# Optimization experiments

Hardware: AMD Instinct MI355X
Metric: run time of the kernel (lower is better)

## Reference

```python
import jax, jax.numpy as jnp
import numpy as np

N, E, D, H, C = 50000, 800000, 64, 2, 64


def setup_inputs() -> dict:
    key = jax.random.key(0)
    ks = jax.random.split(key, 16)
    sc = 1.0 / np.sqrt(D)
    return {
        "left_features": jax.random.normal(ks[0], (N, D), jnp.float32),
        "edge_index": jax.random.randint(ks[1], (2, E), 0, N, jnp.int32),
        "edge_features": jax.random.normal(ks[2], (E, D), jnp.float32),
        "right_features": jax.random.normal(ks[3], (N, D), jnp.float32),
        "scatter_out_size": N,
        # GATConv params (shared lin for src/dst since in_channels is int)
        "W_lin": jax.random.normal(ks[4], (D, H * C), jnp.float32) * sc,
        "att_src": jax.random.normal(ks[5], (H, C), jnp.float32) * sc,
        "att_dst": jax.random.normal(ks[6], (H, C), jnp.float32) * sc,
        "W_edge": jax.random.normal(ks[7], (D, H * C), jnp.float32) * sc,
        "att_edge": jax.random.normal(ks[8], (H, C), jnp.float32) * sc,
        "bias_conv": jnp.zeros((H * C,), jnp.float32),
        # trailing dense layers
        "W_lt": jax.random.normal(ks[9], (H * C, C), jnp.float32) * sc,
        "b_lt": jnp.zeros((C,), jnp.float32),
        "W_fm": jax.random.normal(ks[10], (C, C), jnp.float32) * sc,
        "b_fm": jnp.zeros((C,), jnp.float32),
        "W_pc": jax.random.normal(ks[11], (2 * C, C), jnp.float32) * sc,
        "b_pc": jnp.zeros((C,), jnp.float32),
    }


def reference(left_features, edge_index, edge_features, right_features,
              scatter_out_size, W_lin, att_src, att_dst, W_edge, att_edge,
              bias_conv, W_lt, b_lt, W_fm, b_fm, W_pc, b_pc):
    src, dst = edge_index[0], edge_index[1]
    Nl = scatter_out_size
    # linear projections to [*, H, C]
    x_src = (right_features @ W_lin).reshape(-1, H, C)
    x_dst = (left_features @ W_lin).reshape(-1, H, C)
    # per-node attention logits [*, H]
    a_src = (x_src * att_src).sum(-1)
    a_dst = (x_dst * att_dst).sum(-1)
    e_feat = (edge_features @ W_edge).reshape(-1, H, C)
    a_edge = (e_feat * att_edge).sum(-1)  # [E, H]
    # per-edge logits, leaky relu, segment softmax over dst neighborhoods
    alpha = a_src[src] + a_dst[dst] + a_edge  # [E, H]
    alpha = jax.nn.leaky_relu(alpha, negative_slope=0.2)
    m = jax.ops.segment_max(alpha, dst, num_segments=Nl)
    m = jnp.where(jnp.isfinite(m), m, 0.0)  # empty segments -> 0
    ex = jnp.exp(alpha - m[dst])
    s = jax.ops.segment_sum(ex, dst, num_segments=Nl)
    att = ex / (s[dst] + 1e-16)  # [E, H]
    # weighted message scatter-sum, concat heads
    msg = x_src[src] * att[:, :, None]  # [E, H, C]
    out = jax.ops.segment_sum(msg, dst, num_segments=Nl).reshape(Nl, H * C)
    out = out + bias_conv
    # trailing dense chain
    x = jax.nn.relu(out) @ W_lt + b_lt          # linear_transform
    x = jax.nn.relu(x) @ W_fm + b_fm            # feature_module_final
    left_updated = jnp.concatenate([left_features, x], axis=-1) @ W_pc + b_pc
    return left_updated, edge_index, att
```

## Files before the change

kernel.cpp:

```cpp
#include <hip/hip_runtime.h>
#include <hip/hip_bf16.h>

typedef unsigned int uint32;
typedef unsigned short ushort16;
typedef float f32x4 __attribute__((ext_vector_type(4)));
typedef short bf16x8 __attribute__((ext_vector_type(8)));

#define HH 2
#define CC 64
#define DD 64
#define HC 128

__device__ __forceinline__ float bf2f(ushort16 u) {
    union { float f; uint32 u; } x; x.u = ((uint32)u) << 16; return x.f;
}
__device__ __forceinline__ ushort16 f2bf(float f) {
    union { float f; uint32 u; } x; x.f = f;
    uint32 u = x.u;
    u += 0x7FFFu + ((u >> 16) & 1u);
    return (ushort16)(u >> 16);
}
__device__ __forceinline__ int clampi(int v, int N) {
    return min(max(v, 0), N - 1);
}
__device__ __forceinline__ void cvt_hilo8(const float* x, bf16x8& hi, bf16x8& lo) {
    #pragma unroll
    for (int i = 0; i < 8; i++) {
        union { float f; uint32 u; } a; a.f = x[i];
        uint32 uh = a.u & 0xFFFF0000u;
        hi[i] = (short)(uh >> 16);
        union { float f; uint32 u; } hf; hf.u = uh;
        lo[i] = (short)f2bf(a.f - hf.f);
    }
}

__global__ void k_fold(const float* W_lin, const float* att_src,
                       const float* att_dst, const float* W_edge,
                       const float* att_edge, float* vfold) {
    int t = threadIdx.x;
    int h = t >> 6, d = t & 63;
    float vs = 0.f, vd = 0.f, ve = 0.f;
    for (int c = 0; c < CC; c++) {
        float wl = W_lin[d * HC + h * CC + c];
        vs += wl * att_src[h * CC + c];
        vd += wl * att_dst[h * CC + c];
        ve += W_edge[d * HC + h * CC + c] * att_edge[h * CC + c];
    }
    vfold[t] = vs; vfold[128 + t] = vd; vfold[256 + t] = ve;
}

__global__ __launch_bounds__(256) void k_node_logits(
    const float* right, const float* left, const float* vfold,
    float* a_src, float* a_dst, int N)
{
    __shared__ float vs[HC], vd[HC];
    if (threadIdx.x < HC) {
        vs[threadIdx.x] = vfold[threadIdx.x];
        vd[threadIdx.x] = vfold[HC + threadIdx.x];
    }
    __syncthreads();
    int n = blockIdx.x * 256 + threadIdx.x;
    if (n >= N) return;
    const float4* rr = (const float4*)(right + (size_t)n * DD);
    const float4* lr = (const float4*)(left  + (size_t)n * DD);
    float p0 = 0.f, p1 = 0.f, q0 = 0.f, q1 = 0.f;
    #pragma unroll
    for (int i = 0; i < 16; i++) {
        float4 r4 = rr[i], l4 = lr[i];
        float4 s0 = *(const float4*)&vs[i * 4];
        float4 s1 = *(const float4*)&vs[64 + i * 4];
        float4 d0 = *(const float4*)&vd[i * 4];
        float4 d1 = *(const float4*)&vd[64 + i * 4];
        p0 += r4.x * s0.x + r4.y * s0.y + r4.z * s0.z + r4.w * s0.w;
        p1 += r4.x * s1.x + r4.y * s1.y + r4.z * s1.z + r4.w * s1.w;
        q0 += l4.x * d0.x + l4.y * d0.y + l4.z * d0.z + l4.w * d0.w;
        q1 += l4.x * d1.x + l4.y * d1.y + l4.z * d1.z + l4.w * d1.w;
    }
    *(float2*)(a_src + (size_t)n * 2) = make_float2(p0, p1);
    *(float2*)(a_dst + (size_t)n * 2) = make_float2(q0, q1);
}

__global__ __launch_bounds__(256) void k_edge_alpha(
    const float* edge_feat, const int* ei, const float* vfold,
    const float* a_src, const float* a_dst,
    float* att_slot, int* counts, int E, int N)
{
    __shared__ float vE[HC];
    if (threadIdx.x < HC) vE[threadIdx.x] = vfold[256 + threadIdx.x];
    __syncthreads();
    int e = blockIdx.x * 256 + threadIdx.x;
    if (e >= E) return;
    const float4* row = (const float4*)(edge_feat + (size_t)e * DD);
    float p0 = 0.f, p1 = 0.f;
    #pragma unroll
    for (int i = 0; i < 16; i++) {
        float4 f = row[i];
        float4 w0 = *(const float4*)&vE[i * 4];
        float4 w1 = *(const float4*)&vE[64 + i * 4];
        p0 += f.x * w0.x + f.y * w0.y + f.z * w0.z + f.w * w0.w;
        p1 += f.x * w1.x + f.y * w1.y + f.z * w1.z + f.w * w1.w;
    }
    int s  = clampi(ei[e], N);
    int d2 = clampi(ei[E + e], N);
    float2 asr = *(const float2*)(a_src + (size_t)s * 2);
    float2 ads = *(const float2*)(a_dst + (size_t)d2 * 2);
    float al0 = asr.x + ads.x + p0;
    float al1 = asr.y + ads.y + p1;
    al0 = (al0 > 0.f) ? al0 : 0.2f * al0;
    al1 = (al1 > 0.f) ? al1 : 0.2f * al1;
    *(float2*)(att_slot + (size_t)e * 2) = make_float2(al0, al1);
    atomicAdd(&counts[d2], 1);
}

__global__ void k_scan1(const int* counts, int* bsum, int N) {
    int idx = blockIdx.x * 256 + threadIdx.x;
    int v = (idx < N) ? counts[idx] : 0;
    #pragma unroll
    for (int m = 32; m >= 1; m >>= 1) v += __shfl_xor(v, m, 64);
    __shared__ int wsum[4];
    if ((threadIdx.x & 63) == 0) wsum[threadIdx.x >> 6] = v;
    __syncthreads();
    if (threadIdx.x == 0) bsum[blockIdx.x] = wsum[0] + wsum[1] + wsum[2] + wsum[3];
}

__global__ void k_scan2(const int* bsum, int* bpre, int NB) {
    __shared__ int sh[256];
    int t = threadIdx.x;
    int v = (t < NB) ? bsum[t] : 0;
    sh[t] = v;
    __syncthreads();
    for (int off = 1; off < 256; off <<= 1) {
        int add = (t >= off) ? sh[t - off] : 0;
        __syncthreads();
        sh[t] += add;
        __syncthreads();
    }
    if (t < NB) bpre[t] = sh[t] - v;
}

__global__ void k_scan3(const int* counts, const int* bpre,
                        int* offs, int* cursor, int N) {
    __shared__ int sh[256];
    int t = threadIdx.x;
    int idx = blockIdx.x * 256 + t;
    int v = (idx < N) ? counts[idx] : 0;
    sh[t] = v;
    __syncthreads();
    for (int off = 1; off < 256; off <<= 1) {
        int add = (t >= off) ? sh[t - off] : 0;
        __syncthreads();
        sh[t] += add;
        __syncthreads();
    }
    if (idx < N) {
        int ex = bpre[blockIdx.x] + sh[t] - v;
        offs[idx] = ex;
        cursor[idx] = ex;
    }
}

__global__ void k_ids(const int* ei, int* cursor, int* sorted, int E, int N) {
    int e = blockIdx.x * 256 + threadIdx.x;
    if (e >= E) return;
    int d = clampi(ei[E + e], N);
    int pos = atomicAdd(&cursor[d], 1);
    sorted[pos] = e;
}

__global__ __launch_bounds__(256) void k_gather(
    const int* ei, const int* offs, const int* counts, const int* sorted,
    const float* right, float* att_slot, float* agg, int N)
{
    int w = threadIdx.x >> 6, lane = threadIdx.x & 63;
    int g = lane >> 4, sub = lane & 15;
    for (int n = blockIdx.x * 4 + w; n < N; n += gridDim.x * 4) {
        int start = offs[n], deg = counts[n];
        float m0 = -1e30f, m1 = -1e30f;
        for (int i = lane; i < deg; i += 64) {
            int e = sorted[start + i];
            float2 a = *(const float2*)(att_slot + (size_t)e * 2);
            m0 = fmaxf(m0, a.x);
            m1 = fmaxf(m1, a.y);
        }
        #pragma unroll
        for (int m = 32; m >= 1; m >>= 1) {
            m0 = fmaxf(m0, __shfl_xor(m0, m, 64));
            m1 = fmaxf(m1, __shfl_xor(m1, m, 64));
        }
        float s0 = 0.f, s1 = 0.f;
        f32x4 acc0 = {0.f, 0.f, 0.f, 0.f}, acc1 = {0.f, 0.f, 0.f, 0.f};
        for (int base = 0; base < deg; base += 4) {
            int i = base + g;
            if (i < deg) {
                int e = sorted[start + i];
                float2 a = *(const float2*)(att_slot + (size_t)e * 2);
                float ex0 = __expf(a.x - m0);
                float ex1 = __expf(a.y - m1);
                int si = clampi(ei[e], N);
                f32x4 v = *(const f32x4*)(right + (size_t)si * DD + sub * 4);
                acc0 += ex0 * v;
                acc1 += ex1 * v;
                s0 += ex0; s1 += ex1;
            }
        }
        s0 += __shfl_xor(s0, 16, 64); s0 += __shfl_xor(s0, 32, 64);
        s1 += __shfl_xor(s1, 16, 64); s1 += __shfl_xor(s1, 32, 64);
        #pragma unroll
        for (int j = 0; j < 4; j++) {
            acc0[j] += __shfl_xor(acc0[j], 16, 64);
            acc0[j] += __shfl_xor(acc0[j], 32, 64);
            acc1[j] += __shfl_xor(acc1[j], 16, 64);
            acc1[j] += __shfl_xor(acc1[j], 32, 64);
        }
        float inv0 = 1.f / (s0 + 1e-16f), inv1 = 1.f / (s1 + 1e-16f);
        for (int i = lane; i < deg; i += 64) {
            int e = sorted[start + i];
            float2 a = *(const float2*)(att_slot + (size_t)e * 2);
            a.x = __expf(a.x - m0) * inv0;
            a.y = __expf(a.y - m1) * inv1;
            *(float2*)(att_slot + (size_t)e * 2) = a;
        }
        if (g == 0) {
            f32x4 o = acc0 * inv0;
            *(f32x4*)(agg + (size_t)n * HC + sub * 4) = o;
        } else if (g == 1) {
            f32x4 o = acc1 * inv1;
            *(f32x4*)(agg + (size_t)n * HC + 64 + sub * 4) = o;
        }
    }
}

__global__ __launch_bounds__(256) void k_lin_mfma(
    const float* __restrict__ W_lin, const float* __restrict__ bc,
    float* agg, int N)
{
    __shared__ __align__(16) ushort16 sW[16][512];
    __shared__ float sB[HC];
    for (int t = threadIdx.x; t < 16 * 64; t += 256) {
        int lane = t & 63, f = t >> 6;
        int nt = f & 3, kt = (f >> 2) & 1, h = f >> 3;
        int n = h * CC + nt * 16 + (lane & 15);
        int k0 = kt * 32 + (lane >> 4) * 8;
        #pragma unroll
        for (int i = 0; i < 8; i++)
            sW[f][lane * 8 + i] = f2bf(W_lin[(size_t)(k0 + i) * HC + n]);
    }
    if (threadIdx.x < HC) sB[threadIdx.x] = bc[threadIdx.x];
    __syncthreads();
    int w = threadIdx.x >> 6, lane = threadIdx.x & 63;
    int lhi = lane >> 4, llo = lane & 15;
    int tiles = (N + 63) >> 6;
    for (int tile = blockIdx.x; tile < tiles; tile += gridDim.x) {
        int nb = tile * 64 + w * 16;
        int arow = min(nb + llo, N - 1);
        const float* ap = agg + (size_t)arow * HC;
        bf16x8 Ah[2][2], Al[2][2];
        #pragma unroll
        for (int h = 0; h < 2; h++)
            #pragma unroll
            for (int kt = 0; kt < 2; kt++) {
                float x8[8];
                *(f32x4*)&x8[0] = *(const f32x4*)(ap + h * 64 + kt * 32 + lhi * 8);
                *(f32x4*)&x8[4] = *(const f32x4*)(ap + h * 64 + kt * 32 + lhi * 8 + 4);
                cvt_hilo8(x8, Ah[h][kt], Al[h][kt]);
            }
        f32x4 acc[2][4];
        #pragma unroll
        for (int h = 0; h < 2; h++)
            #pragma unroll
            for (int nt = 0; nt < 4; nt++) {
                float b = sB[h * 64 + nt * 16 + llo];
                acc[h][nt][0] = b; acc[h][nt][1] = b;
                acc[h][nt][2] = b; acc[h][nt][3] = b;
            }
        #pragma unroll
        for (int h = 0; h < 2; h++)
            #pragma unroll
            for (int kt = 0; kt < 2; kt++)
                #pragma unroll
                for (int nt = 0; nt < 4; nt++) {
                    bf16x8 b = *(const bf16x8*)&sW[h * 8 + kt * 4 + nt][lane * 8];
                    acc[h][nt] = __builtin_amdgcn_mfma_f32_16x16x32_bf16(Al[h][kt], b, acc[h][nt], 0, 0, 0);
                    acc[h][nt] = __builtin_amdgcn_mfma_f32_16x16x32_bf16(Ah[h][kt], b, acc[h][nt], 0, 0, 0);
                }
        #pragma unroll
        for (int h = 0; h < 2; h++)
            #pragma unroll
            for (int nt = 0; nt < 4; nt++)
                #pragma unroll
                for (int j = 0; j < 4; j++) {
                    int node = nb + 4 * lhi + j;
                    if (node < N)
                        agg[(size_t)node * HC + h * 64 + nt * 16 + llo] =
                            fmaxf(acc[h][nt][j], 0.f);
                }
    }
}

__global__ __launch_bounds__(256) void k_tail_mfma(
    const float* __restrict__ t0, const float* __restrict__ left,
    const float* __restrict__ W_lt, const float* __restrict__ b_lt,
    const float* __restrict__ W_fm, const float* __restrict__ b_fm,
    const float* __restrict__ W_pc, const float* __restrict__ b_pc,
    float* __restrict__ out, int N)
{
    __shared__ __align__(16) ushort16 sWlt[16][512];
    __shared__ __align__(16) ushort16 sWfm[8][512];
    __shared__ __align__(16) ushort16 sWpT[8][512];
    __shared__ __align__(16) ushort16 sWpB[8][512];
    __shared__ __align__(16) float sX[4][1024];
    __shared__ float sblt[CC], sbfm[CC], sbpc[CC];
    for (int t = threadIdx.x; t < 16 * 64; t += 256) {
        int lane = t & 63, f = t >> 6, nt = f & 3, kt = f >> 2;
        int n = nt * 16 + (lane & 15), k0 = kt * 32 + (lane >> 4) * 8;
        #pragma unroll
        for (int i = 0; i < 8; i++)
            sWlt[f][lane * 8 + i] = f2bf(W_lt[(k0 + i) * CC + n]);
    }
    for (int t = threadIdx.x; t < 8 * 64; t += 256) {
        int lane = t & 63, f = t >> 6, nt = f & 3, kt = f >> 2;
        int n = nt * 16 + (lane & 15), k0 = kt * 32 + (lane >> 4) * 8;
        #pragma unroll
        for (int i = 0; i < 8; i++) {
            sWfm[f][lane * 8 + i] = f2bf(W_fm[(k0 + i) * CC + n]);
            sWpT[f][lane * 8 + i] = f2bf(W_pc[(k0 + i) * CC + n]);
            sWpB[f][lane * 8 + i] = f2bf(W_pc[(64 + k0 + i) * CC + n]);
        }
    }
    if (threadIdx.x < CC) {
        sblt[threadIdx.x] = b_lt[threadIdx.x];
        sbfm[threadIdx.x] = b_fm[threadIdx.x];
        sbpc[threadIdx.x] = b_pc[threadIdx.x];
    }
    __syncthreads();
    int w = threadIdx.x >> 6, lane = threadIdx.x & 63;
    int lhi = lane >> 4, llo = lane & 15;
    float* xw = &sX[w][0];
    int swz = (llo & 7) << 2;
    int tiles = (N + 63) >> 6;
    for (int tile = blockIdx.x; tile < tiles; tile += gridDim.x) {
        int nb = tile * 64 + w * 16;
        int arow = min(nb + llo, N - 1);
        f32x4 acc2[4];
        #pragma unroll
        for (int nt = 0; nt < 4; nt++) {
            float b = sblt[nt * 16 + llo];
            acc2[nt][0] = b; acc2[nt][1] = b; acc2[nt][2] = b; acc2[nt][3] = b;
        }
        const float* tp = t0 + (size_t)arow * HC;
        #pragma unroll
        for (int kt = 0; kt < 4; kt++) {
            float x8[8];
            *(f32x4*)&x8[0] = *(const f32x4*)(tp + kt * 32 + lhi * 8);
            *(f32x4*)&x8[4] = *(const f32x4*)(tp + kt * 32 + lhi * 8 + 4);
            bf16x8 ah, al; cvt_hilo8(x8, ah, al);
            #pragma unroll
            for (int nt = 0; nt < 4; nt++) {
                bf16x8 b = *(const bf16x8*)&sWlt[kt * 4 + nt][lane * 8];
                acc2[nt] = __builtin_amdgcn_mfma_f32_16x16x32_bf16(al, b, acc2[nt], 0, 0, 0);
                acc2[nt] = __builtin_amdgcn_mfma_f32_16x16x32_bf16(ah, b, acc2[nt], 0, 0, 0);
            }
        }
        #pragma unroll
        for (int nt = 0; nt < 4; nt++)
            #pragma unroll
            for (int j = 0; j < 4; j++) {
                int row = 4 * lhi + j, col = nt * 16 + llo;
                xw[row * 64 + (col ^ ((row & 7) << 2))] = fmaxf(acc2[nt][j], 0.f);
            }
        f32x4 acc3[4];
        #pragma unroll
        for (int nt = 0; nt < 4; nt++) {
            float b = sbfm[nt * 16 + llo];
            acc3[nt][0] = b; acc3[nt][1] = b; acc3[nt][2] = b; acc3[nt][3] = b;
        }
        #pragma unroll
        for (int kt = 0; kt < 2; kt++) {
            int k0 = kt * 32 + lhi * 8;
            float x8[8];
            *(f32x4*)&x8[0] = *(const f32x4*)&xw[llo * 64 + ((k0    ) ^ swz)];
            *(f32x4*)&x8[4] = *(const f32x4*)&xw[llo * 64 + ((k0 + 4) ^ swz)];
            bf16x8 ah, al; cvt_hilo8(x8, ah, al);
            #pragma unroll
            for (int nt = 0; nt < 4; nt++) {
                bf16x8 b = *(const bf16x8*)&sWfm[kt * 4 + nt][lane * 8];
                acc3[nt] = __builtin_amdgcn_mfma_f32_16x16x32_bf16(al, b, acc3[nt], 0, 0, 0);
                acc3[nt] = __builtin_amdgcn_mfma_f32_16x16x32_bf16(ah, b, acc3[nt], 0, 0, 0);
            }
        }
        #pragma unroll
        for (int nt = 0; nt < 4; nt++)
            #pragma unroll
            for (int j = 0; j < 4; j++) {
                int row = 4 * lhi + j, col = nt * 16 + llo;
                xw[row * 64 + (col ^ ((row & 7) << 2))] = acc3[nt][j];
            }
        f32x4 acc4[4];
        #pragma unroll
        for (int nt = 0; nt < 4; nt++) {
            float b = sbpc[nt * 16 + llo];
            acc4[nt][0] = b; acc4[nt][1] = b; acc4[nt][2] = b; acc4[nt][3] = b;
        }
        const float* lp = left + (size_t)arow * DD;
        #pragma unroll
        for (int kt = 0; kt < 2; kt++) {
            float x8[8];
            *(f32x4*)&x8[0] = *(const f32x4*)(lp + kt * 32 + lhi * 8);
            *(f32x4*)&x8[4] = *(const f32x4*)(lp + kt * 32 + lhi * 8 + 4);
            bf16x8 ah, al; cvt_hilo8(x8, ah, al);
            #pragma unroll
            for (int nt = 0; nt < 4; nt++) {
                bf16x8 b = *(const bf16x8*)&sWpT[kt * 4 + nt][lane * 8];
                acc4[nt] = __builtin_amdgcn_mfma_f32_16x16x32_bf16(al, b, acc4[nt], 0, 0, 0);
                acc4[nt] = __builtin_amdgcn_mfma_f32_16x16x32_bf16(ah, b, acc4[nt], 0, 0, 0);
            }
        }
        #pragma unroll
        for (int kt = 0; kt < 2; kt++) {
            int k0 = kt * 32 + lhi * 8;
            float x8[8];
            *(f32x4*)&x8[0] = *(const f32x4*)&xw[llo * 64 + ((k0    ) ^ swz)];
            *(f32x4*)&x8[4] = *(const f32x4*)&xw[llo * 64 + ((k0 + 4) ^ swz)];
            bf16x8 ah, al; cvt_hilo8(x8, ah, al);
            #pragma unroll
            for (int nt = 0; nt < 4; nt++) {
                bf16x8 b = *(const bf16x8*)&sWpB[kt * 4 + nt][lane * 8];
                acc4[nt] = __builtin_amdgcn_mfma_f32_16x16x32_bf16(al, b, acc4[nt], 0, 0, 0);
                acc4[nt] = __builtin_amdgcn_mfma_f32_16x16x32_bf16(ah, b, acc4[nt], 0, 0, 0);
            }
        }
        #pragma unroll
        for (int nt = 0; nt < 4; nt++)
            #pragma unroll
            for (int j = 0; j < 4; j++) {
                int node = nb + 4 * lhi + j;
                if (node < N)
                    out[(size_t)node * CC + nt * 16 + llo] = acc4[nt][j];
            }
    }
}

__global__ void k_copy_idx(const int* ei, float* out, int n) {
    for (int i = blockIdx.x * blockDim.x + threadIdx.x; i < n;
         i += gridDim.x * blockDim.x)
        out[i] = (float)ei[i];
}

extern "C" void kernel_launch(void* const* d_in, const int* in_sizes, int n_in,
                              void* d_out, int out_size, void* d_ws, size_t ws_size,
                              hipStream_t stream) {
    const float* left      = (const float*)d_in[0];
    const int*   ei        = (const int*)d_in[1];
    const float* efeat     = (const float*)d_in[2];
    const float* right     = (const float*)d_in[3];
    const float* W_lin     = (const float*)d_in[5];
    const float* att_src   = (const float*)d_in[6];
    const float* att_dst   = (const float*)d_in[7];
    const float* W_edge    = (const float*)d_in[8];
    const float* att_edge  = (const float*)d_in[9];
    const float* bias_conv = (const float*)d_in[10];
    const float* W_lt      = (const float*)d_in[11];
    const float* b_lt      = (const float*)d_in[12];
    const float* W_fm      = (const float*)d_in[13];
    const float* b_fm      = (const float*)d_in[14];
    const float* W_pc      = (const float*)d_in[15];
    const float* b_pc      = (const float*)d_in[16];

    const int N = in_sizes[0] / DD;
    const int E = in_sizes[2] / DD;
    const int NB = (N + 255) / 256;

    float* ws     = (float*)d_ws;
    float* vfold  = ws;
    float* a_src  = ws + 512;
    float* a_dst  = a_src + 2 * (size_t)N;
    int*   counts = (int*)(a_dst + 2 * (size_t)N);
    int*   offs   = counts + N;
    int*   cursor = offs + N;
    int*   bsum   = cursor + N;
    int*   bpre   = bsum + 256;
    int*   sorted = bpre + 256;
    float* agg    = (float*)(sorted + E);
    (void)ws_size; (void)n_in; (void)out_size;

    float* out_lu   = (float*)d_out;
    float* out_ei   = out_lu + (size_t)N * CC;
    float* att_slot = out_ei + (size_t)2 * E;

    hipMemsetAsync(counts, 0, (size_t)N * sizeof(int), stream);

    hipLaunchKernelGGL(k_fold, dim3(1), dim3(128), 0, stream,
                       W_lin, att_src, att_dst, W_edge, att_edge, vfold);
    hipLaunchKernelGGL(k_node_logits, dim3((N + 255) / 256), dim3(256), 0, stream,
                       right, left, vfold, a_src, a_dst, N);
    hipLaunchKernelGGL(k_edge_alpha, dim3((E + 255) / 256), dim3(256), 0, stream,
                       efeat, ei, vfold, a_src, a_dst, att_slot, counts, E, N);
    hipLaunchKernelGGL(k_scan1, dim3(NB), dim3(256), 0, stream,
                       counts, bsum, N);
    hipLaunchKernelGGL(k_scan2, dim3(1), dim3(256), 0, stream,
                       bsum, bpre, NB);
    hipLaunchKernelGGL(k_scan3, dim3(NB), dim3(256), 0, stream,
                       counts, bpre, offs, cursor, N);
    hipLaunchKernelGGL(k_ids, dim3((E + 255) / 256), dim3(256), 0, stream,
                       ei, cursor, sorted, E, N);
    hipLaunchKernelGGL(k_gather, dim3((N + 3) / 4), dim3(256), 0, stream,
                       ei, offs, counts, sorted, right, att_slot, agg, N);
    hipLaunchKernelGGL(k_lin_mfma, dim3(512), dim3(256), 0, stream,
                       W_lin, bias_conv, agg, N);
    hipLaunchKernelGGL(k_tail_mfma, dim3(512), dim3(256), 0, stream,
                       agg, left, W_lt, b_lt, W_fm, b_fm, W_pc, b_pc, out_lu, N);
    hipLaunchKernelGGL(k_copy_idx, dim3(1024), dim3(256), 0, stream,
                       ei, out_ei, 2 * E);
}
```

Baseline: 541.1 us.

## Coalesce row dot-products, use online-softmax gather, fuse index copy into edge kernel

Node and edge logit kernels now split each 64-float row across 16 lanes with shuffle reductions. Each thread previously walked a whole row, so neighbouring lanes read addresses 256 bytes apart and loads were uncoalesced. The gather kernel now gives each node a 16-lane group that does a single-pass online softmax, replacing the separate max pass and the 4-way edge split per wavefront. The edge_index float copy moves into the edge kernel, removing one launch. The cost is a serial per-neighbour loop with extra exps per edge and fewer lanes per node, which could hurt latency hiding on high-degree nodes.

```diff
diff --git a/kernel.cpp b/kernel.cpp
--- a/kernel.cpp
+++ b/kernel.cpp
@@ -22,6 +22,9 @@
 }
 __device__ __forceinline__ int clampi(int v, int N) {
     return min(max(v, 0), N - 1);
+}
+__device__ __forceinline__ float dot4(f32x4 a, f32x4 b) {
+    return a.x * b.x + a.y * b.y + a.z * b.z + a.w * b.w;
 }
 __device__ __forceinline__ void cvt_hilo8(const float* x, bf16x8& hi, bf16x8& lo) {
     #pragma unroll
@@ -59,57 +62,68 @@
         vd[threadIdx.x] = vfold[HC + threadIdx.x];
     }
     __syncthreads();
-    int n = blockIdx.x * 256 + threadIdx.x;
-    if (n >= N) return;
-    const float4* rr = (const float4*)(right + (size_t)n * DD);
-    const float4* lr = (const float4*)(left  + (size_t)n * DD);
-    float p0 = 0.f, p1 = 0.f, q0 = 0.f, q1 = 0.f;
+    int g = threadIdx.x >> 4, sub = threadIdx.x & 15;
+    f32x4 s0 = *(const f32x4*)&vs[sub * 4];
+    f32x4 s1 = *(const f32x4*)&vs[64 + sub * 4];
+    f32x4 d0 = *(const f32x4*)&vd[sub * 4];
+    f32x4 d1 = *(const f32x4*)&vd[64 + sub * 4];
     #pragma unroll
-    for (int i = 0; i < 16; i++) {
-        float4 r4 = rr[i], l4 = lr[i];
-        float4 s0 = *(const float4*)&vs[i * 4];
-        float4 s1 = *(const float4*)&vs[64 + i * 4];
-        float4 d0 = *(const float4*)&vd[i * 4];
-        float4 d1 = *(const float4*)&vd[64 + i * 4];
-        p0 += r4.x * s0.x + r4.y * s0.y + r4.z * s0.z + r4.w * s0.w;
-        p1 += r4.x * s1.x + r4.y * s1.y + r4.z * s1.z + r4.w * s1.w;
-        q0 += l4.x * d0.x + l4.y * d0.y + l4.z * d0.z + l4.w * d0.w;
-        q1 += l4.x * d1.x + l4.y * d1.y + l4.z * d1.z + l4.w * d1.w;
-    }
-    *(float2*)(a_src + (size_t)n * 2) = make_float2(p0, p1);
-    *(float2*)(a_dst + (size_t)n * 2) = make_float2(q0, q1);
+    for (int it = 0; it < 4; it++) {
+        int n = blockIdx.x * 64 + it * 16 + g;
+        if (n >= N) break;
+        f32x4 r4 = *(const f32x4*)(right + (size_t)n * DD + sub * 4);
+        f32x4 l4 = *(const f32x4*)(left  + (size_t)n * DD + sub * 4);
+        float p0 = dot4(r4, s0), p1 = dot4(r4, s1);
+        float q0 = dot4(l4, d0), q1 = dot4(l4, d1);
+        #pragma unroll
+        for (int m = 8; m >= 1; m >>= 1) {
+            p0 += __shfl_xor(p0, m, 64); p1 += __shfl_xor(p1, m, 64);
+            q0 += __shfl_xor(q0, m, 64); q1 += __shfl_xor(q1, m, 64);
+        }
+        if (sub == 0) {
+            *(float2*)(a_src + (size_t)n * 2) = make_float2(p0, p1);
+            *(float2*)(a_dst + (size_t)n * 2) = make_float2(q0, q1);
+        }
+    }
 }
 
 __global__ __launch_bounds__(256) void k_edge_alpha(
     const float* edge_feat, const int* ei, const float* vfold,
     const float* a_src, const float* a_dst,
-    float* att_slot, int* counts, int E, int N)
+    float* att_slot, int* counts, float* out_ei, int E, int N)
 {
     __shared__ float vE[HC];
     if (threadIdx.x < HC) vE[threadIdx.x] = vfold[256 + threadIdx.x];
     __syncthreads();
-    int e = blockIdx.x * 256 + threadIdx.x;
-    if (e >= E) return;
-    const float4* row = (const float4*)(edge_feat + (size_t)e * DD);
-    float p0 = 0.f, p1 = 0.f;
+    int g = threadIdx.x >> 4, sub = threadIdx.x & 15;
+    f32x4 w0 = *(const f32x4*)&vE[sub * 4];
+    f32x4 w1 = *(const f32x4*)&vE[64 + sub * 4];
     #pragma unroll
-    for (int i = 0; i < 16; i++) {
-        float4 f = row[i];
-        float4 w0 = *(const float4*)&vE[i * 4];
-        float4 w1 = *(const float4*)&vE[64 + i * 4];
-        p0 += f.x * w0.x + f.y * w0.y + f.z * w0.z + f.w * w0.w;
-        p1 += f.x * w1.x + f.y * w1.y + f.z * w1.z + f.w * w1.w;
-    }
-    int s  = clampi(ei[e], N);
-    int d2 = clampi(ei[E + e], N);
-    float2 asr = *(const float2*)(a_src + (size_t)s * 2);
-    float2 ads = *(const float2*)(a_dst + (size_t)d2 * 2);
-    float al0 = asr.x + ads.x + p0;
-    float al1 = asr.y + ads.y + p1;
-    al0 = (al0 > 0.f) ? al0 : 0.2f * al0;
-    al1 = (al1 > 0.f) ? al1 : 0.2f * al1;
-    *(float2*)(att_slot + (size_t)e * 2) = make_float2(al0, al1);
-    atomicAdd(&counts[d2], 1);
+    for (int it = 0; it < 4; it++) {
+        int e = blockIdx.x * 64 + it * 16 + g;
+        if (e >= E) break;
+        f32x4 f = *(const f32x4*)(edge_feat + (size_t)e * DD + sub * 4);
+        float p0 = dot4(f, w0), p1 = dot4(f, w1);
+        #pragma unroll
+        for (int m = 8; m >= 1; m >>= 1) {
+            p0 += __shfl_xor(p0, m, 64); p1 += __shfl_xor(p1, m, 64);
+        }
+        if (sub == 0) {
+            int raw_s = ei[e], raw_d = ei[E + e];
+            int s  = clampi(raw_s, N);
+            int d2 = clampi(raw_d, N);
+            float2 asr = *(const float2*)(a_src + (size_t)s * 2);
+            float2 ads = *(const float2*)(a_dst + (size_t)d2 * 2);
+            float al0 = asr.x + ads.x + p0;
+            float al1 = asr.y + ads.y + p1;
+            al0 = (al0 > 0.f) ? al0 : 0.2f * al0;
+            al1 = (al1 > 0.f) ? al1 : 0.2f * al1;
+            *(float2*)(att_slot + (size_t)e * 2) = make_float2(al0, al1);
+            atomicAdd(&counts[d2], 1);
+            out_ei[e]     = (float)raw_s;
+            out_ei[E + e] = (float)raw_d;
+        }
+    }
 }
 
 __global__ void k_scan1(const int* counts, int* bsum, int N) {
@@ -171,63 +185,35 @@
     const int* ei, const int* offs, const int* counts, const int* sorted,
     const float* right, float* att_slot, float* agg, int N)
 {
-    int w = threadIdx.x >> 6, lane = threadIdx.x & 63;
-    int g = lane >> 4, sub = lane & 15;
-    for (int n = blockIdx.x * 4 + w; n < N; n += gridDim.x * 4) {
-        int start = offs[n], deg = counts[n];
-        float m0 = -1e30f, m1 = -1e30f;
-        for (int i = lane; i < deg; i += 64) {
-            int e = sorted[start + i];
-            float2 a = *(const float2*)(att_slot + (size_t)e * 2);
-            m0 = fmaxf(m0, a.x);
-            m1 = fmaxf(m1, a.y);
-        }
-        #pragma unroll
-        for (int m = 32; m >= 1; m >>= 1) {
-            m0 = fmaxf(m0, __shfl_xor(m0, m, 64));
-            m1 = fmaxf(m1, __shfl_xor(m1, m, 64));
-        }
-        float s0 = 0.f, s1 = 0.f;
-        f32x4 acc0 = {0.f, 0.f, 0.f, 0.f}, acc1 = {0.f, 0.f, 0.f, 0.f};
-        for (int base = 0; base < deg; base += 4) {
-            int i = base + g;
-            if (i < deg) {
-                int e = sorted[start + i];
-                float2 a = *(const float2*)(att_slot + (size_t)e * 2);
-                float ex0 = __expf(a.x - m0);
-                float ex1 = __expf(a.y - m1);
-                int si = clampi(ei[e], N);
-                f32x4 v = *(const f32x4*)(right + (size_t)si * DD + sub * 4);
-                acc0 += ex0 * v;
-                acc1 += ex1 * v;
-                s0 += ex0; s1 += ex1;
-            }
-        }
-        s0 += __shfl_xor(s0, 16, 64); s0 += __shfl_xor(s0, 32, 64);
-        s1 += __shfl_xor(s1, 16, 64); s1 += __shfl_xor(s1, 32, 64);
-        #pragma unroll
-        for (int j = 0; j < 4; j++) {
-            acc0[j] += __shfl_xor(acc0[j], 16, 64);
-            acc0[j] += __shfl_xor(acc0[j], 32, 64);
-            acc1[j] += __shfl_xor(acc1[j], 16, 64);
-            acc1[j] += __shfl_xor(acc1[j], 32, 64);
-        }
-        float inv0 = 1.f / (s0 + 1e-16f), inv1 = 1.f / (s1 + 1e-16f);
-        for (int i = lane; i < deg; i += 64) {
-            int e = sorted[start + i];
-            float2 a = *(const float2*)(att_slot + (size_t)e * 2);
-            a.x = __expf(a.x - m0) * inv0;
-            a.y = __expf(a.y - m1) * inv1;
-            *(float2*)(att_slot + (size_t)e * 2) = a;
-        }
-        if (g == 0) {
-            f32x4 o = acc0 * inv0;
-            *(f32x4*)(agg + (size_t)n * HC + sub * 4) = o;
-        } else if (g == 1) {
-            f32x4 o = acc1 * inv1;
-            *(f32x4*)(agg + (size_t)n * HC + 64 + sub * 4) = o;
-        }
-    }
+    int g = threadIdx.x >> 4, sub = threadIdx.x & 15;
+    int n = blockIdx.x * 16 + g;
+    if (n >= N) return;
+    int start = offs[n], deg = counts[n];
+    float m0 = -1e30f, m1 = -1e30f, s0 = 0.f, s1 = 0.f;
+    f32x4 acc0 = {0.f, 0.f, 0.f, 0.f}, acc1 = {0.f, 0.f, 0.f, 0.f};
+    for (int i = 0; i < deg; i++) {
+        int e = sorted[start + i];
+        float2 a = *(const float2*)(att_slot + (size_t)e * 2);
+        int si = clampi(ei[e], N);
+        float nm0 = fmaxf(m0, a.x), nm1 = fmaxf(m1, a.y);
+        float f0 = __expf(m0 - nm0), f1 = __expf(m1 - nm1);
+        float e0 = __expf(a.x - nm0), e1 = __expf(a.y - nm1);
+        f32x4 v = *(const f32x4*)(right + (size_t)si * DD + sub * 4);
+        s0 = s0 * f0 + e0;  s1 = s1 * f1 + e1;
+        acc0 = acc0 * f0 + e0 * v;
+        acc1 = acc1 * f1 + e1 * v;
+        m0 = nm0; m1 = nm1;
+    }
+    float inv0 = 1.f / (s0 + 1e-16f), inv1 = 1.f / (s1 + 1e-16f);
+    for (int i = sub; i < deg; i += 16) {
+        int e = sorted[start + i];
+        float2 a = *(const float2*)(att_slot + (size_t)e * 2);
+        a.x = __expf(a.x - m0) * inv0;
+        a.y = __expf(a.y - m1) * inv1;
+        *(float2*)(att_slot + (size_t)e * 2) = a;
+    }
+    *(f32x4*)(agg + (size_t)n * HC + sub * 4)      = acc0 * inv0;
+    *(f32x4*)(agg + (size_t)n * HC + 64 + sub * 4) = acc1 * inv1;
 }
 
 __global__ __launch_bounds__(256) void k_lin_mfma(
@@ -440,12 +426,6 @@
     }
 }
 
-__global__ void k_copy_idx(const int* ei, float* out, int n) {
-    for (int i = blockIdx.x * blockDim.x + threadIdx.x; i < n;
-         i += gridDim.x * blockDim.x)
-        out[i] = (float)ei[i];
-}
-
 extern "C" void kernel_launch(void* const* d_in, const int* in_sizes, int n_in,
                               void* d_out, int out_size, void* d_ws, size_t ws_size,
                               hipStream_t stream) {
@@ -461,8 +441,8 @@
     const float* bias_conv = (const float*)d_in[10];
     const float* W_lt      = (const float*)d_in[11];
     const float* b_lt      = (const float*)d_in[12];
+    const float* b_fm      = (const float*)d_in[14];
     const float* W_fm      = (const float*)d_in[13];
-    const float* b_fm      = (const float*)d_in[14];
     const float* W_pc      = (const float*)d_in[15];
     const float* b_pc      = (const float*)d_in[16];
 
@@ -491,10 +471,11 @@
 
     hipLaunchKernelGGL(k_fold, dim3(1), dim3(128), 0, stream,
                        W_lin, att_src, att_dst, W_edge, att_edge, vfold);
-    hipLaunchKernelGGL(k_node_logits, dim3((N + 255) / 256), dim3(256), 0, stream,
+    hipLaunchKernelGGL(k_node_logits, dim3((N + 63) / 64), dim3(256), 0, stream,
                        right, left, vfold, a_src, a_dst, N);
-    hipLaunchKernelGGL(k_edge_alpha, dim3((E + 255) / 256), dim3(256), 0, stream,
-                       efeat, ei, vfold, a_src, a_dst, att_slot, counts, E, N);
+    hipLaunchKernelGGL(k_edge_alpha, dim3((E + 63) / 64), dim3(256), 0, stream,
+                       efeat, ei, vfold, a_src, a_dst, att_slot, counts, out_ei,
+                       E, N);
     hipLaunchKernelGGL(k_scan1, dim3(NB), dim3(256), 0, stream,
                        counts, bsum, N);
     hipLaunchKernelGGL(k_scan2, dim3(1), dim3(256), 0, stream,
@@ -503,12 +484,10 @@
                        counts, bpre, offs, cursor, N);
     hipLaunchKernelGGL(k_ids, dim3((E + 255) / 256), dim3(256), 0, stream,
                        ei, cursor, sorted, E, N);
-    hipLaunchKernelGGL(k_gather, dim3((N + 3) / 4), dim3(256), 0, stream,
+    hipLaunchKernelGGL(k_gather, dim3((N + 15) / 16), dim3(256), 0, stream,
                        ei, offs, counts, sorted, right, att_slot, agg, N);
     hipLaunchKernelGGL(k_lin_mfma, dim3(512), dim3(256), 0, stream,
                        W_lin, bias_conv, agg, N);
     hipLaunchKernelGGL(k_tail_mfma, dim3(512), dim3(256), 0, stream,
                        agg, left, W_lt, b_lt, W_fm, b_fm, W_pc, b_pc, out_lu, N);
-    hipLaunchKernelGGL(k_copy_idx, dim3(1024), dim3(256), 0, stream,
-                       ei, out_ei, 2 * E);
-}
+}
```

Result: faster. 525.8 us (-2.8%).
